# Kernel tuning notes

Hardware: AMD Instinct MI355X
Metric: run time of the kernel (lower is better)

Reference implementation:

```python
import jax, jax.numpy as jnp
import numpy as np

B, S, D = 1, 2048, 2048
NH, NKV, HD = 32, 8, 64
D_FIBER, D_CONTROL = 16, 64
ALPHA = 0.995  # ema_momentum
NEG = -1e9


def setup_inputs() -> dict:
    key = jax.random.key(0)
    ks = jax.random.split(key, 10)
    hidden_states = jax.random.normal(ks[0], (B, S, D), dtype=jnp.float32)
    # causal additive mask [1,1,S,S]
    causal = jnp.tril(jnp.ones((S, S), dtype=bool))
    attention_mask = jnp.where(causal, 0.0, NEG).astype(jnp.float32)[None, None]
    # RoPE tables [S, HD]
    inv_freq = 1.0 / (10000.0 ** (np.arange(0, HD, 2, dtype=np.float32) / HD))
    pos = np.arange(S, dtype=np.float32)
    freqs = pos[:, None] * inv_freq[None, :]
    emb = np.concatenate([freqs, freqs], axis=-1)
    cos = jnp.asarray(np.cos(emb), dtype=jnp.float32)
    sin = jnp.asarray(np.sin(emb), dtype=jnp.float32)
    # adapter params
    Wf = 0.02 * jax.random.normal(ks[1], (D, D_FIBER), dtype=jnp.float32)
    W1 = jax.random.normal(ks[2], (D + D_FIBER, D_CONTROL), dtype=jnp.float32) * (2.0 / (D + D_FIBER + D_CONTROL)) ** 0.5
    b1 = jnp.zeros((D_CONTROL,), dtype=jnp.float32)
    W2 = jax.random.normal(ks[3], (D_CONTROL, 1), dtype=jnp.float32) * (2.0 / (D_CONTROL + 1)) ** 0.5
    b2 = 0.1 * jax.random.normal(ks[4], (1,), dtype=jnp.float32)
    gate_scale = jnp.float32(0.5)
    # attention projections (Llama-style, no bias); stored as [in, out]
    s = 1.0 / np.sqrt(D)
    Wq = s * jax.random.normal(ks[5], (D, NH * HD), dtype=jnp.float32)
    Wk = s * jax.random.normal(ks[6], (D, NKV * HD), dtype=jnp.float32)
    Wv = s * jax.random.normal(ks[7], (D, NKV * HD), dtype=jnp.float32)
    Wo = s * jax.random.normal(ks[8], (NH * HD, D), dtype=jnp.float32)
    return dict(hidden_states=hidden_states, attention_mask=attention_mask,
                cos=cos, sin=sin, Wf=Wf, W1=W1, b1=b1, W2=W2, b2=b2,
                gate_scale=gate_scale, Wq=Wq, Wk=Wk, Wv=Wv, Wo=Wo)


def _rotate_half(x):
    x1, x2 = jnp.split(x, 2, axis=-1)
    return jnp.concatenate([-x2, x1], axis=-1)


def reference(hidden_states, attention_mask, cos, sin, Wf, W1, b1, W2, b2,
              gate_scale, Wq, Wk, Wv, Wo):
    h = hidden_states.astype(jnp.float32)  # [B,S,D]
    # ---- CFAdapter ----
    fiber = h @ Wf                                      # [B,S,d_fiber]
    combined = jnp.concatenate([h, fiber], axis=-1)     # [B,S,D+d_fiber]
    hmid = jax.nn.gelu(combined @ W1 + b1, approximate=False)
    risk = (hmid @ W2 + b2)[..., 0]                     # [B,S]
    field = (1.0 - ALPHA) * risk                        # prev_field is None
    f_mean = field.mean(axis=1, keepdims=True)
    f_std = field.std(axis=1, keepdims=True, ddof=1) + 1e-6  # torch unbiased std
    gate = (field - f_mean) / f_std                     # [B,S]
    # ---- attention with inline RoPE + gate bias ----
    q = (h @ Wq).reshape(B, S, NH, HD).transpose(0, 2, 1, 3)   # [B,NH,S,HD]
    k = (h @ Wk).reshape(B, S, NKV, HD).transpose(0, 2, 1, 3)  # [B,NKV,S,HD]
    v = (h @ Wv).reshape(B, S, NKV, HD).transpose(0, 2, 1, 3)
    q = q * cos + _rotate_half(q) * sin
    k = k * cos + _rotate_half(k) * sin
    n_rep = NH // NKV
    k = jnp.repeat(k, n_rep, axis=1)  # repeat_interleave semantics
    v = jnp.repeat(v, n_rep, axis=1)
    scores = jnp.einsum('bhqd,bhkd->bhqk', q, k) / jnp.sqrt(jnp.float32(HD))
    scores = scores + attention_mask + gate_scale * gate[:, None, None, :]
    attn = jax.nn.softmax(scores.astype(jnp.float32), axis=-1).astype(q.dtype)
    out = jnp.einsum('bhqk,bhkd->bhqd', attn, v)
    out = out.transpose(0, 2, 1, 3).reshape(B, S, NH * HD)
    out = out @ Wo
    return out
```

## Files before the change

kernel.cpp:

```cpp
#include <hip/hip_runtime.h>

#define S_LEN 2048
#define D_DIM 2048
#define NHEAD 32
#define NKVH  8
#define HDIM  64
#define NBT   3200

typedef __attribute__((ext_vector_type(4))) float f32x4;
typedef __attribute__((ext_vector_type(8))) short bf16x8;

__device__ __forceinline__ unsigned short f2bf(float x) {
    union { float f; unsigned u; } v; v.f = x;
    unsigned r = v.u + 0x7FFFu + ((v.u >> 16) & 1u);
    return (unsigned short)(r >> 16);
}

#define GLD(gsrc, ldst) __builtin_amdgcn_global_load_lds( \
    (const __attribute__((address_space(1))) unsigned int*)(const void*)(gsrc), \
    (__attribute__((address_space(3))) unsigned int*)(void*)(ldst), 16, 0, 0)

#define SWZ(r) (((r) & 7) << 4)

#define KPERM(kk) (((kk) & 32) | (((kk) & 12) << 1) | (((kk) & 16) >> 2) | ((kk) & 3))

__device__ __forceinline__ void dev_trans(const float* __restrict__ W, unsigned short* __restrict__ WT,
                                          int N, int k0, int n0, int t, unsigned short L[64][65]) {
    for (int it = 0; it < 16; ++it) {
        int e = it * 256 + t;
        int r = e >> 6, c = e & 63;
        L[c][r] = f2bf(W[(size_t)(k0 + r) * N + n0 + c]);
    }
    __syncthreads();
    for (int it = 0; it < 16; ++it) {
        int e = it * 256 + t;
        int n = e >> 6, kk = e & 63;
        WT[(size_t)(n0 + n) * 2048 + k0 + kk] = L[n][kk];
    }
}

__global__ __launch_bounds__(256) void k_prep(const float* __restrict__ h, unsigned short* __restrict__ hb,
        const float* __restrict__ Wq, const float* __restrict__ Wk, const float* __restrict__ Wv,
        const float* __restrict__ Wo, const float* __restrict__ Wf, const float* __restrict__ W1,
        unsigned short* __restrict__ bt, unsigned short* __restrict__ wot) {
    __shared__ unsigned short L[64][65];
    int b = blockIdx.x, t = threadIdx.x;
    if (b < 4096) {
        int i = (b * 256 + t) * 4;
        float4 v = *(const float4*)(h + i);
        ushort4 o;
        o.x = f2bf(v.x); o.y = f2bf(v.y); o.z = f2bf(v.z); o.w = f2bf(v.w);
        *(ushort4*)(hb + i) = o;
    } else if (b < 5120) {
        int bb = b - 4096;
        dev_trans(Wq, bt, 2048, (bb & 31) * 64, (bb >> 5) * 64, t, L);
    } else if (b < 5376) {
        int bb = b - 5120;
        dev_trans(Wk, bt + (size_t)2048 * 2048, 512, (bb & 31) * 64, (bb >> 5) * 64, t, L);
    } else if (b < 5632) {
        int bb = b - 5376;
        dev_trans(Wv, bt + (size_t)2560 * 2048, 512, (bb & 31) * 64, (bb >> 5) * 64, t, L);
    } else if (b < 6656) {
        int bb = b - 5632;
        dev_trans(Wo, wot, 2048, (bb & 31) * 64, (bb >> 5) * 64, t, L);
    } else if (b < 6688) {
        int k0 = (b - 6656) * 64;
        for (int it = 0; it < 4; ++it) {
            int e = it * 256 + t;
            int r = e >> 4, c = e & 15;
            L[c][r] = f2bf(Wf[(size_t)(k0 + r) * 16 + c]);
        }
        __syncthreads();
        unsigned short* dst = bt + (size_t)3072 * 2048;
        for (int it = 0; it < 4; ++it) {
            int e = it * 256 + t;
            int c = e >> 6, kk = e & 63;
            dst[(size_t)c * 2048 + k0 + kk] = L[c][kk];
        }
    } else if (b < 6720) {
        int k0 = (b - 6688) * 64;
        dev_trans(W1, bt + (size_t)3088 * 2048, 64, k0, 0, t, L);
    } else {
        int bb = b - 6720;
        unsigned* p = (unsigned*)(bt + (size_t)3152 * 2048);
        p[bb * 256 + t] = 0u;
    }
}

__global__ __launch_bounds__(256) void k_fuse_vtrans(const float* __restrict__ adcols,
                        const float* __restrict__ W1, const float* __restrict__ b1,
                        const float* __restrict__ W2, const float* __restrict__ b2,
                        float* __restrict__ field,
                        const unsigned short* __restrict__ vrow, unsigned short* __restrict__ vt) {
    __shared__ unsigned short L[64][65];
    int b = blockIdx.x, t = threadIdx.x;
    if (b < 512) {
        int wv = t >> 6, l = t & 63;
        int s = b * 4 + wv;
        const float* row = adcols + (size_t)s * 128;
        float x = row[16 + l] + b1[l];
#pragma unroll
        for (int f = 0; f < 16; ++f) x += row[f] * W1[(size_t)(2048 + f) * 64 + l];
        float hm = 0.5f * x * (1.f + erff(x * 0.70710678118654752f));
        float p = hm * W2[l];
        for (int m = 32; m; m >>= 1) p += __shfl_xor(p, m);
        if (l == 0) field[s] = 0.005f * (p + b2[0]);
    } else {
        int bb = b - 512;
        int s0 = (bb & 31) * 64, hk = bb >> 5;
        for (int it = 0; it < 16; ++it) {
            int e = it * 256 + t;
            int r = e >> 6, c = e & 63;
            L[c][r] = vrow[(size_t)(s0 + r) * 512 + hk * 64 + c];
        }
        __syncthreads();
        for (int it = 0; it < 16; ++it) {
            int e = it * 256 + t;
            int c = e >> 6, kk = e & 63;
            vt[((size_t)hk * 64 + c) * S_LEN + s0 + KPERM(kk)] = L[c][kk];
        }
    }
}

__global__ void k_gate(const float* __restrict__ field, float* __restrict__ gate) {
    __shared__ float red[256];
    int t = threadIdx.x;
    float s = 0.f;
    for (int i = t; i < S_LEN; i += 256) s += field[i];
    red[t] = s; __syncthreads();
    for (int w = 128; w; w >>= 1) { if (t < w) red[t] += red[t + w]; __syncthreads(); }
    float mean = red[0] / (float)S_LEN;
    __syncthreads();
    float v = 0.f;
    for (int i = t; i < S_LEN; i += 256) { float d = field[i] - mean; v += d * d; }
    red[t] = v; __syncthreads();
    for (int w = 128; w; w >>= 1) { if (t < w) red[t] += red[t + w]; __syncthreads(); }
    float stdv = sqrtf(red[0] / (float)(S_LEN - 1)) + 1e-6f;
    for (int i = t; i < S_LEN; i += 256) gate[i] = (field[i] - mean) / stdv;
}

__device__ __forceinline__ void gemm_core(const unsigned short* __restrict__ A,
                                          const unsigned short* __restrict__ BT,
                                          int K, int m0, int n0,
                                          char* As, char* Bs,
                                          int wr, int wc, int lr, int lkb,
                                          f32x4 acc[2][4]) {
    int t = threadIdx.x;
    int wv = t >> 6;
    int srow = t >> 3;
    int scol = 8 * ((t & 7) ^ (srow & 7));
    const unsigned short* Ag = A + (size_t)(m0 + srow) * K + scol;
    const unsigned short* Bg = BT + (size_t)(n0 + srow) * K + scol;
    char* lA = As + wv * 1024;
    char* lB = Bs + wv * 1024;
    int nk = K / 64;
    GLD(Ag, lA); GLD(Ag + (size_t)32 * K, lA + 4096);
    GLD(Bg, lB); GLD(Bg + (size_t)32 * K, lB + 4096);
    GLD(Bg + (size_t)64 * K, lB + 8192); GLD(Bg + (size_t)96 * K, lB + 12288);
    for (int kt = 0; kt < nk; ++kt) {
        __syncthreads();
        bf16x8 af[2][2], bfv[4][2];
#pragma unroll
        for (int i = 0; i < 2; ++i) {
            int row = wr + i * 16 + lr;
#pragma unroll
            for (int kh = 0; kh < 2; ++kh)
                af[i][kh] = *(const bf16x8*)(As + row * 128 + ((kh * 64 + lkb) ^ SWZ(row)));
        }
#pragma unroll
        for (int j = 0; j < 4; ++j) {
            int row = wc + j * 16 + lr;
#pragma unroll
            for (int kh = 0; kh < 2; ++kh)
                bfv[j][kh] = *(const bf16x8*)(Bs + row * 128 + ((kh * 64 + lkb) ^ SWZ(row)));
        }
#pragma unroll
        for (int kh = 0; kh < 2; ++kh)
#pragma unroll
            for (int i = 0; i < 2; ++i)
#pragma unroll
                for (int j = 0; j < 4; ++j)
                    acc[i][j] = __builtin_amdgcn_mfma_f32_16x16x32_bf16(af[i][kh], bfv[j][kh], acc[i][j], 0, 0, 0);
        __syncthreads();
        if (kt + 1 < nk) {
            const unsigned short* Ak = Ag + (size_t)(kt + 1) * 64;
            const unsigned short* Bk = Bg + (size_t)(kt + 1) * 64;
            GLD(Ak, lA); GLD(Ak + (size_t)32 * K, lA + 4096);
            GLD(Bk, lB); GLD(Bk + (size_t)32 * K, lB + 4096);
            GLD(Bk + (size_t)64 * K, lB + 8192); GLD(Bk + (size_t)96 * K, lB + 12288);
        }
    }
}

__global__ __launch_bounds__(256) void k_gemm_qkv(const unsigned short* __restrict__ A,
                                                  const unsigned short* __restrict__ BT,
                                                  const float* __restrict__ cs,
                                                  const float* __restrict__ sn,
                                                  unsigned short* __restrict__ qb,
                                                  unsigned short* __restrict__ kbuf,
                                                  unsigned short* __restrict__ vrow,
                                                  float* __restrict__ adcols) {
    __shared__ __align__(16) char As[8192];
    __shared__ __align__(16) char Bs[16384];
    const int K = 2048;
    int flat = blockIdx.y * gridDim.x + blockIdx.x;
    int cpx = (gridDim.x * gridDim.y) >> 3;
    int swz = (flat & 7) * cpx + (flat >> 3);
    int m0 = (swz / gridDim.x) * 64, n0 = (swz % gridDim.x) * 128;
    int t = threadIdx.x;
    int wv = t >> 6, ln = t & 63;
    int wr = (wv >> 1) * 32, wc = (wv & 1) * 64;
    int lr = ln & 15, lkb = (ln >> 4) * 16;
    f32x4 acc[2][4] = {};
    gemm_core(A, BT, K, m0, n0, As, Bs, wr, wc, lr, lkb, acc);
    int orow = (ln >> 4) * 4;
    int col0 = n0 + wc;
    if (col0 < 2560) {
        bool isq = (col0 < 2048);
        unsigned short* dst = isq ? qb : kbuf;
        int hh = (isq ? col0 : col0 - 2048) >> 6;
        float qscale = isq ? 0.125f : 1.0f;
#pragma unroll
        for (int i = 0; i < 2; ++i)
#pragma unroll
            for (int r = 0; r < 4; ++r) {
                int s = m0 + wr + i * 16 + orow + r;
#pragma unroll
                for (int j = 0; j < 4; ++j) {
                    int d = j * 16 + lr;
                    float c = cs[s * 64 + d], si = sn[s * 64 + d];
                    float val = acc[i][j][r];
                    float prt = acc[i][j ^ 2][r];
                    float out = val * c + ((j < 2) ? -prt : prt) * si;
                    dst[((size_t)hh * S_LEN + s) * 64 + d] = f2bf(out * qscale);
                }
            }
    } else if (col0 < 3072) {
        int vc0 = col0 - 2560;
#pragma unroll
        for (int i = 0; i < 2; ++i)
#pragma unroll
            for (int j = 0; j < 4; ++j) {
                unsigned short* vp = vrow + (size_t)(m0 + wr + i * 16 + orow) * 512 + vc0 + j * 16 + lr;
                for (int r = 0; r < 4; ++r) vp[(size_t)r * 512] = f2bf(acc[i][j][r]);
            }
    } else {
        int ac0 = col0 - 3072;
#pragma unroll
        for (int i = 0; i < 2; ++i)
#pragma unroll
            for (int j = 0; j < 4; ++j) {
                float* ap = adcols + (size_t)(m0 + wr + i * 16 + orow) * 128 + ac0 + j * 16 + lr;
                for (int r = 0; r < 4; ++r) ap[(size_t)r * 128] = acc[i][j][r];
            }
    }
}

__global__ __launch_bounds__(256) void k_gemm(const unsigned short* __restrict__ A,
                                              const unsigned short* __restrict__ BT,
                                              float* __restrict__ C, int M, int N, int K) {
    __shared__ __align__(16) char As[8192];
    __shared__ __align__(16) char Bs[16384];
    int flat = blockIdx.y * gridDim.x + blockIdx.x;
    int cpx = (gridDim.x * gridDim.y) >> 3;
    int swz = (flat & 7) * cpx + (flat >> 3);
    int m0 = (swz / gridDim.x) * 64, n0 = (swz % gridDim.x) * 128;
    int t = threadIdx.x;
    int wv = t >> 6, ln = t & 63;
    int wr = (wv >> 1) * 32, wc = (wv & 1) * 64;
    int lr = ln & 15, lkb = (ln >> 4) * 16;
    f32x4 acc[2][4] = {};
    gemm_core(A, BT, K, m0, n0, As, Bs, wr, wc, lr, lkb, acc);
    int orow = (ln >> 4) * 4;
#pragma unroll
    for (int i = 0; i < 2; ++i)
#pragma unroll
        for (int j = 0; j < 4; ++j) {
            float* Cp = C + (size_t)(m0 + wr + i * 16 + orow) * N + n0 + wc + j * 16 + lr;
            for (int r = 0; r < 4; ++r) Cp[(size_t)r * N] = acc[i][j][r];
        }
}

__device__ __forceinline__ bf16x8 packP(const f32x4& a, const f32x4& b) {
    union { unsigned u[4]; bf16x8 v; } pk;
    asm("v_cvt_pk_bf16_f32 %0, %1, %2" : "=v"(pk.u[0]) : "v"(a[0]), "v"(a[1]));
    asm("v_cvt_pk_bf16_f32 %0, %1, %2" : "=v"(pk.u[1]) : "v"(a[2]), "v"(a[3]));
    asm("v_cvt_pk_bf16_f32 %0, %1, %2" : "=v"(pk.u[2]) : "v"(b[0]), "v"(b[1]));
    asm("v_cvt_pk_bf16_f32 %0, %1, %2" : "=v"(pk.u[3]) : "v"(b[2]), "v"(b[3]));
    return pk.v;
}

__global__ __launch_bounds__(128, 2) void k_attn(const unsigned short* __restrict__ qb,
                                                 const unsigned short* __restrict__ kb,
                                                 const unsigned short* __restrict__ vt,
                                                 const float* __restrict__ gate,
                                                 const float* __restrict__ gs_p,
                                                 unsigned short* __restrict__ attnout) {
    __shared__ __align__(16) char Kl[2][8192];
    __shared__ __align__(16) char Vl[2][8192];
    int h = blockIdx.y, hk = h >> 2;
    int qt = (h < 16) ? (31 - blockIdx.x) : blockIdx.x;
    int t = threadIdx.x, wv = t >> 6, l = t & 63;
    int lq = l & 15, lg = l >> 4;
    float gs = gs_p[0];
    int q0 = qt * 64 + wv * 32;
    const unsigned short* qbase = qb + ((size_t)h * S_LEN + q0) * 64;
    bf16x8 aq[2][2];
#pragma unroll
    for (int qf = 0; qf < 2; ++qf)
#pragma unroll
        for (int hf = 0; hf < 2; ++hf)
            aq[qf][hf] = *(const bf16x8*)(qbase + (qf * 16 + lq) * 64 + hf * 32 + lg * 8);
    f32x4 o[2][4] = {};
    float m_[2] = { -INFINITY, -INFINITY };
    float ls_[2] = { 0.f, 0.f };
    int nkt = qt + 1;
    int srow = t >> 3;
    int scol = 8 * ((t & 7) ^ (srow & 7));
    const unsigned short* kg = kb + (size_t)hk * S_LEN * 64;
    const unsigned short* vg = vt + (size_t)hk * 64 * S_LEN;
    char* lKb0 = Kl[0] + wv * 1024; char* lKb1 = Kl[1] + wv * 1024;
    char* lVb0 = Vl[0] + wv * 1024; char* lVb1 = Vl[1] + wv * 1024;
#define STAGE_KV(K0, DK, DV) do { \
        GLD(kg + (size_t)((K0) + srow) * 64 + scol, (DK)); \
        GLD(kg + (size_t)((K0) + 16 + srow) * 64 + scol, (DK) + 2048); \
        GLD(kg + (size_t)((K0) + 32 + srow) * 64 + scol, (DK) + 4096); \
        GLD(kg + (size_t)((K0) + 48 + srow) * 64 + scol, (DK) + 6144); \
        GLD(vg + (size_t)srow * S_LEN + (K0) + scol, (DV)); \
        GLD(vg + (size_t)(16 + srow) * S_LEN + (K0) + scol, (DV) + 2048); \
        GLD(vg + (size_t)(32 + srow) * S_LEN + (K0) + scol, (DV) + 4096); \
        GLD(vg + (size_t)(48 + srow) * S_LEN + (K0) + scol, (DV) + 6144); \
    } while (0)
    STAGE_KV(0, lKb0, lVb0);
    for (int kt = 0; kt < nkt; ++kt) {
        __syncthreads();
        if (kt + 1 < nkt) {
            int k0n = (kt + 1) * 64;
            char* dK = ((kt + 1) & 1) ? lKb1 : lKb0;
            char* dV = ((kt + 1) & 1) ? lVb1 : lVb0;
            STAGE_KV(k0n, dK, dV);
        }
        int k0 = kt * 64;
        bool diag = (kt == nkt - 1);
        const char* Kb = Kl[kt & 1];
        const char* Vb = Vl[kt & 1];
        f32x4 sc[2][4] = {};
#pragma unroll
        for (int ct = 0; ct < 4; ++ct) {
            int krow = ct * 16 + lq;
#pragma unroll
            for (int hf = 0; hf < 2; ++hf) {
                bf16x8 bk = *(const bf16x8*)(Kb + krow * 128 + ((hf * 64 + lg * 16) ^ SWZ(krow)));
#pragma unroll
                for (int qf = 0; qf < 2; ++qf)
                    sc[qf][ct] = __builtin_amdgcn_mfma_f32_16x16x32_bf16(bk, aq[qf][hf], sc[qf][ct], 0, 0, 0);
            }
        }
        float vmax[2] = { -INFINITY, -INFINITY };
#pragma unroll
        for (int ct = 0; ct < 4; ++ct) {
            f32x4 g4 = *(const f32x4*)(gate + k0 + ct * 16 + lg * 4);
#pragma unroll
            for (int qf = 0; qf < 2; ++qf) {
                int q = q0 + qf * 16 + lq;
#pragma unroll
                for (int r = 0; r < 4; ++r) {
                    float val = sc[qf][ct][r] + gs * g4[r];
                    if (diag && (k0 + ct * 16 + lg * 4 + r > q)) val = -1e9f;
                    sc[qf][ct][r] = val;
                    vmax[qf] = fmaxf(vmax[qf], val);
                }
            }
        }
#pragma unroll
        for (int qf = 0; qf < 2; ++qf) {
            vmax[qf] = fmaxf(vmax[qf], __shfl_xor(vmax[qf], 16));
            vmax[qf] = fmaxf(vmax[qf], __shfl_xor(vmax[qf], 32));
        }
        bool cond = (vmax[0] <= m_[0] + 8.f) && (vmax[1] <= m_[1] + 8.f);
        if (!__all(cond)) {
#pragma unroll
            for (int qf = 0; qf < 2; ++qf) {
                float mn = fmaxf(m_[qf], vmax[qf]);
                float scl = __expf(m_[qf] - mn);
                ls_[qf] *= scl;
#pragma unroll
                for (int dt = 0; dt < 4; ++dt) o[qf][dt] *= scl;
                m_[qf] = mn;
            }
        }
#pragma unroll
        for (int qf = 0; qf < 2; ++qf)
#pragma unroll
            for (int ct = 0; ct < 4; ++ct)
#pragma unroll
                for (int r = 0; r < 4; ++r) {
                    float p = __expf(sc[qf][ct][r] - m_[qf]);
                    sc[qf][ct][r] = p;
                    ls_[qf] += p;
                }
#pragma unroll
        for (int ks = 0; ks < 2; ++ks) {
            bf16x8 pf0 = packP(sc[0][2 * ks], sc[0][2 * ks + 1]);
            bf16x8 pf1 = packP(sc[1][2 * ks], sc[1][2 * ks + 1]);
#pragma unroll
            for (int dt = 0; dt < 4; ++dt) {
                int vr = dt * 16 + lq;
                bf16x8 bv = *(const bf16x8*)(Vb + vr * 128 + ((ks * 64 + lg * 16) ^ SWZ(vr)));
                o[0][dt] = __builtin_amdgcn_mfma_f32_16x16x32_bf16(bv, pf0, o[0][dt], 0, 0, 0);
                o[1][dt] = __builtin_amdgcn_mfma_f32_16x16x32_bf16(bv, pf1, o[1][dt], 0, 0, 0);
            }
        }
    }
#undef STAGE_KV
#pragma unroll
    for (int qf = 0; qf < 2; ++qf) {
        float s = ls_[qf];
        s += __shfl_xor(s, 16);
        s += __shfl_xor(s, 32);
        float inv = 1.f / s;
        int q = q0 + qf * 16 + lq;
        unsigned short* orow = attnout + (size_t)q * 2048 + h * 64;
#pragma unroll
        for (int dt = 0; dt < 4; ++dt) {
            ushort4 st;
            st.x = f2bf(o[qf][dt][0] * inv); st.y = f2bf(o[qf][dt][1] * inv);
            st.z = f2bf(o[qf][dt][2] * inv); st.w = f2bf(o[qf][dt][3] * inv);
            *(ushort4*)(orow + dt * 16 + lg * 4) = st;
        }
    }
}

extern "C" void kernel_launch(void* const* d_in, const int* in_sizes, int n_in,
                              void* d_out, int out_size, void* d_ws, size_t ws_size,
                              hipStream_t stream) {
    const float* h    = (const float*)d_in[0];
    const float* cosT = (const float*)d_in[2];
    const float* sinT = (const float*)d_in[3];
    const float* Wf   = (const float*)d_in[4];
    const float* W1   = (const float*)d_in[5];
    const float* b1   = (const float*)d_in[6];
    const float* W2   = (const float*)d_in[7];
    const float* b2   = (const float*)d_in[8];
    const float* gs   = (const float*)d_in[9];
    const float* Wq   = (const float*)d_in[10];
    const float* Wk   = (const float*)d_in[11];
    const float* Wv   = (const float*)d_in[12];
    const float* Wo   = (const float*)d_in[13];
    float* out = (float*)d_out;

    char* ws = (char*)d_ws;
    unsigned short* hb     = (unsigned short*)(ws);
    unsigned short* bt     = (unsigned short*)(ws + 8388608);
    unsigned short* qbuf   = (unsigned short*)(ws + 21495808);
    unsigned short* kbuf   = (unsigned short*)(ws + 29884416);
    unsigned short* vrow   = (unsigned short*)(ws + 31981568);
    float*          adcols = (float*)(ws + 34078720);
    float*          field  = (float*)(ws + 35127296);
    float*          gate   = (float*)(ws + 35135488);
    unsigned short* wot    = (unsigned short*)(ws + 35143680);
    unsigned short* vt      = (unsigned short*)(ws + 16777216);
    unsigned short* attnout = (unsigned short*)(ws);

    k_prep<<<dim3(6912), dim3(256), 0, stream>>>(h, hb, Wq, Wk, Wv, Wo, Wf, W1, bt, wot);
    k_gemm_qkv<<<dim3(25, 32), dim3(256), 0, stream>>>(hb, bt, cosT, sinT, qbuf, kbuf, vrow, adcols);
    k_fuse_vtrans<<<dim3(768), dim3(256), 0, stream>>>(adcols, W1, b1, W2, b2, field, vrow, vt);
    k_gate<<<dim3(1), dim3(256), 0, stream>>>(field, gate);
    k_attn<<<dim3(32, 32), dim3(128), 0, stream>>>(qbuf, kbuf, vt, gate, gs, attnout);
    k_gemm<<<dim3(16, 32), dim3(256), 0, stream>>>(attnout, wot, out, 2048, 2048, 2048);
}
```

Measured before the change: 156.2 us.

## Split attention KV range into two chunks and merge partials

Each query tile's causal KV range is split into two halves, each handled by a separate block (flash-decoding style split-K). Each block writes unnormalized bf16 partial outputs plus per-row max and sum, and a new merge kernel combines them using log-sum-exp rescaling. This doubles the attention grid to improve occupancy and load balance across CUs. The cost is an extra kernel launch, extra global traffic for the partials, and an added bf16 rounding of the unnormalized partial outputs.

Measured after the change: 172.6 us. +10.5%, slower.

```diff
diff --git a/kernel.cpp b/kernel.cpp
--- a/kernel.cpp
+++ b/kernel.cpp
@@ -14,6 +14,9 @@
     union { float f; unsigned u; } v; v.f = x;
     unsigned r = v.u + 0x7FFFu + ((v.u >> 16) & 1u);
     return (unsigned short)(r >> 16);
+}
+__device__ __forceinline__ float bf2f(unsigned short u) {
+    union { unsigned u; float f; } v; v.u = ((unsigned)u) << 16; return v.f;
 }
 
 #define GLD(gsrc, ldst) __builtin_amdgcn_global_load_lds( \
@@ -295,15 +298,35 @@
                                                  const unsigned short* __restrict__ vt,
                                                  const float* __restrict__ gate,
                                                  const float* __restrict__ gs_p,
-                                                 unsigned short* __restrict__ attnout) {
+                                                 unsigned short* __restrict__ pO0,
+                                                 unsigned short* __restrict__ pO1,
+                                                 float2* __restrict__ pmlA,
+                                                 float2* __restrict__ pmlB) {
     __shared__ __align__(16) char Kl[2][8192];
     __shared__ __align__(16) char Vl[2][8192];
     int h = blockIdx.y, hk = h >> 2;
-    int qt = (h < 16) ? (31 - blockIdx.x) : blockIdx.x;
+    int chunk = blockIdx.x & 1, xt = blockIdx.x >> 1;
+    int qt = (h < 16) ? (31 - xt) : xt;
     int t = threadIdx.x, wv = t >> 6, l = t & 63;
     int lq = l & 15, lg = l >> 4;
+    int q0 = qt * 64 + wv * 32;
+    int nkt_full = qt + 1;
+    int half = nkt_full >> 1;
+    int kt0 = chunk ? half : 0;
+    int kt1 = chunk ? nkt_full : half;
+    unsigned short* pO = chunk ? pO1 : pO0;
+    float2* pml = chunk ? pmlB : pmlA;
+    if (kt0 == kt1) {
+        if (lg == 0) {
+#pragma unroll
+            for (int qf = 0; qf < 2; ++qf) {
+                int q = q0 + qf * 16 + lq;
+                pml[h * 2048 + q] = make_float2(-1e30f, 0.f);
+            }
+        }
+        return;
+    }
     float gs = gs_p[0];
-    int q0 = qt * 64 + wv * 32;
     const unsigned short* qbase = qb + ((size_t)h * S_LEN + q0) * 64;
     bf16x8 aq[2][2];
 #pragma unroll
@@ -314,7 +337,6 @@
     f32x4 o[2][4] = {};
     float m_[2] = { -INFINITY, -INFINITY };
     float ls_[2] = { 0.f, 0.f };
-    int nkt = qt + 1;
     int srow = t >> 3;
     int scol = 8 * ((t & 7) ^ (srow & 7));
     const unsigned short* kg = kb + (size_t)hk * S_LEN * 64;
@@ -331,17 +353,21 @@
         GLD(vg + (size_t)(32 + srow) * S_LEN + (K0) + scol, (DV) + 4096); \
         GLD(vg + (size_t)(48 + srow) * S_LEN + (K0) + scol, (DV) + 6144); \
     } while (0)
-    STAGE_KV(0, lKb0, lVb0);
-    for (int kt = 0; kt < nkt; ++kt) {
+    {
+        char* dK = (kt0 & 1) ? lKb1 : lKb0;
+        char* dV = (kt0 & 1) ? lVb1 : lVb0;
+        STAGE_KV(kt0 * 64, dK, dV);
+    }
+    for (int kt = kt0; kt < kt1; ++kt) {
         __syncthreads();
-        if (kt + 1 < nkt) {
+        if (kt + 1 < kt1) {
             int k0n = (kt + 1) * 64;
             char* dK = ((kt + 1) & 1) ? lKb1 : lKb0;
             char* dV = ((kt + 1) & 1) ? lVb1 : lVb0;
             STAGE_KV(k0n, dK, dV);
         }
         int k0 = kt * 64;
-        bool diag = (kt == nkt - 1);
+        bool diag = (kt == qt);
         const char* Kb = Kl[kt & 1];
         const char* Vb = Vl[kt & 1];
         f32x4 sc[2][4] = {};
@@ -415,20 +441,51 @@
 #undef STAGE_KV
 #pragma unroll
     for (int qf = 0; qf < 2; ++qf) {
-        float s = ls_[qf];
-        s += __shfl_xor(s, 16);
-        s += __shfl_xor(s, 32);
-        float inv = 1.f / s;
+        float lsr = ls_[qf];
+        lsr += __shfl_xor(lsr, 16);
+        lsr += __shfl_xor(lsr, 32);
         int q = q0 + qf * 16 + lq;
-        unsigned short* orow = attnout + (size_t)q * 2048 + h * 64;
+        unsigned short* orow = pO + (size_t)q * 2048 + h * 64;
 #pragma unroll
         for (int dt = 0; dt < 4; ++dt) {
             ushort4 st;
-            st.x = f2bf(o[qf][dt][0] * inv); st.y = f2bf(o[qf][dt][1] * inv);
-            st.z = f2bf(o[qf][dt][2] * inv); st.w = f2bf(o[qf][dt][3] * inv);
+            st.x = f2bf(o[qf][dt][0]); st.y = f2bf(o[qf][dt][1]);
+            st.z = f2bf(o[qf][dt][2]); st.w = f2bf(o[qf][dt][3]);
             *(ushort4*)(orow + dt * 16 + lg * 4) = st;
         }
-    }
+        if (lg == 0) pml[h * 2048 + q] = make_float2(m_[qf], lsr);
+    }
+}
+
+__global__ __launch_bounds__(256) void k_merge(const unsigned short* __restrict__ pO0,
+                                               unsigned short* __restrict__ pO1out,
+                                               const float2* __restrict__ pmlA,
+                                               const float2* __restrict__ pmlB) {
+    int idx8 = blockIdx.x * 256 + threadIdx.x;
+    int q = idx8 >> 8;
+    int col = (idx8 & 255) * 8;
+    int h = col >> 6;
+    float2 a = pmlA[h * 2048 + q];
+    float2 b = pmlB[h * 2048 + q];
+    float m = fmaxf(a.x, b.x);
+    float eA = __expf(a.x - m), eB = __expf(b.x - m);
+    float inv = 1.f / (a.y * eA + b.y * eB);
+    float sA = eA * inv, sB = eB * inv;
+    const unsigned short* pa = pO0 + (size_t)q * 2048 + col;
+    unsigned short* pb = pO1out + (size_t)q * 2048 + col;
+    ushort4 a0 = *(const ushort4*)pa, a1 = *(const ushort4*)(pa + 4);
+    ushort4 b0 = *(const ushort4*)pb, b1 = *(const ushort4*)(pb + 4);
+    ushort4 o0, o1;
+    o0.x = f2bf(bf2f(a0.x) * sA + bf2f(b0.x) * sB);
+    o0.y = f2bf(bf2f(a0.y) * sA + bf2f(b0.y) * sB);
+    o0.z = f2bf(bf2f(a0.z) * sA + bf2f(b0.z) * sB);
+    o0.w = f2bf(bf2f(a0.w) * sA + bf2f(b0.w) * sB);
+    o1.x = f2bf(bf2f(a1.x) * sA + bf2f(b1.x) * sB);
+    o1.y = f2bf(bf2f(a1.y) * sA + bf2f(b1.y) * sB);
+    o1.z = f2bf(bf2f(a1.z) * sA + bf2f(b1.z) * sB);
+    o1.w = f2bf(bf2f(a1.w) * sA + bf2f(b1.w) * sB);
+    *(ushort4*)pb = o0;
+    *(ushort4*)(pb + 4) = o1;
 }
 
 extern "C" void kernel_launch(void* const* d_in, const int* in_sizes, int n_in,
@@ -459,13 +516,18 @@
     float*          field  = (float*)(ws + 35127296);
     float*          gate   = (float*)(ws + 35135488);
     unsigned short* wot    = (unsigned short*)(ws + 35143680);
+    unsigned short* pO1     = (unsigned short*)(ws);
+    unsigned short* pO0     = (unsigned short*)(ws + 8388608);
     unsigned short* vt      = (unsigned short*)(ws + 16777216);
-    unsigned short* attnout = (unsigned short*)(ws);
+    float2*         pmlA    = (float2*)(ws + 43532288);
+    float2*         pmlB    = (float2*)(ws + 44056576);
+    unsigned short* attnout = pO1;
 
     k_prep<<<dim3(6912), dim3(256), 0, stream>>>(h, hb, Wq, Wk, Wv, Wo, Wf, W1, bt, wot);
     k_gemm_qkv<<<dim3(25, 32), dim3(256), 0, stream>>>(hb, bt, cosT, sinT, qbuf, kbuf, vrow, adcols);
     k_fuse_vtrans<<<dim3(768), dim3(256), 0, stream>>>(adcols, W1, b1, W2, b2, field, vrow, vt);
     k_gate<<<dim3(1), dim3(256), 0, stream>>>(field, gate);
-    k_attn<<<dim3(32, 32), dim3(128), 0, stream>>>(qbuf, kbuf, vt, gate, gs, attnout);
+    k_attn<<<dim3(64, 32), dim3(128), 0, stream>>>(qbuf, kbuf, vt, gate, gs, pO0, pO1, pmlA, pmlB);
+    k_merge<<<dim3(2048), dim3(256), 0, stream>>>(pO0, pO1, pmlA, pmlB);
     k_gemm<<<dim3(16, 32), dim3(256), 0, stream>>>(attnout, wot, out, 2048, 2048, 2048);
 }
```
